# Kernel optimization log

Measured on AMD Instinct MI355X. Metric: run time of the kernel, lower is better.

Reference implementation:

```python
import jax, jax.numpy as jnp
import numpy as np

NMS_SIGMA = 2.0
MASK_THRESH = 0.5
N = 500
H = W = 256
NUM_CLS = 80


def setup_inputs() -> dict:
    key = jax.random.key(0)
    k1, k2, k3 = jax.random.split(key, 3)
    mask_preds = jax.random.uniform(k1, (N, H, W), dtype=jnp.float32)
    cate_scores = jax.random.uniform(k2, (N,), dtype=jnp.float32)
    cate_labels = jax.random.randint(k3, (N,), 0, NUM_CLS, dtype=jnp.int32)
    return {"mask_preds": mask_preds, "cate_scores": cate_scores, "cate_labels": cate_labels}


def reference(mask_preds, cate_scores, cate_labels):
    n = mask_preds.shape[0]
    # binarize masks (SOLOv2 inference: seg_masks = seg_preds > mask_thresh)
    seg_masks = (mask_preds > MASK_THRESH).astype(mask_preds.dtype)  # [N,H,W]
    sum_masks = seg_masks.sum(axis=(1, 2))                           # [N]
    # mask scoring: average soft score inside the binary mask
    seg_scores = (mask_preds * seg_masks).sum(axis=(1, 2)) / jnp.maximum(sum_masks, 1.0)
    scores = cate_scores * seg_scores                                # [N]
    # sort descending by score (matrix-NMS assumes sorted order)
    order = jnp.argsort(-scores)
    scores = scores[order]
    labels = cate_labels[order]
    flat = seg_masks[order].reshape(n, -1)                           # [N,HW]
    sums = sum_masks[order]
    # pairwise mask IoU, upper-triangular (j suppressed by i<j)
    inter = flat @ flat.T                                            # [N,N]
    union = sums[:, None] + sums[None, :] - inter
    iou = jnp.triu(inter / jnp.maximum(union, 1.0), k=1)
    label_match = jnp.triu((labels[:, None] == labels[None, :]).astype(iou.dtype), k=1)
    decay_iou = iou * label_match                                    # [N,N]
    # gaussian matrix-NMS decay
    compensate_iou = decay_iou.max(axis=0)                           # [N]
    decay_matrix = jnp.exp(-NMS_SIGMA * (decay_iou ** 2 - compensate_iou[:, None] ** 2))
    coeff = decay_matrix.min(axis=0)                                 # [N]
    updated_scores = scores * coeff
    return updated_scores
```

## Files before the change

kernel.cpp:

```cpp
#include <hip/hip_runtime.h>
#include <cstdint>

typedef unsigned long long u64;

#define THRESH 0.5f
#define SIGMA 2.0f

#define TPB 64
#define NSPLIT 8
#define CH 64
#define CST 66

__global__ __launch_bounds__(256) void k_pack_score(
    const float* __restrict__ preds, u64* __restrict__ packed,
    double* __restrict__ pssum, int* __restrict__ pcnt, int HW)
{
    const int b = blockIdx.x;
    const int i = b >> 2, sub = b & 3;
    const int seg = HW >> 2;
    const float* src = preds + (size_t)i * HW + (size_t)sub * seg;
    u64* dst = packed + (size_t)i * (HW >> 6) + (size_t)sub * (seg >> 6);
    const int tid = threadIdx.x;
    const int wave = tid >> 6, lane = tid & 63;
    double ssum = 0.0;
    int cnt = 0;
    const int iters = seg >> 10;
    for (int k = 0; k < iters; ++k) {
        const int p = (k << 10) + (wave << 8) + (lane << 2);
        const float4 v = *reinterpret_cast<const float4*>(src + p);
        const bool b0 = v.x > THRESH, b1 = v.y > THRESH, b2 = v.z > THRESH, b3 = v.w > THRESH;
        const u64 m0 = __ballot(b0);
        const u64 m1 = __ballot(b1);
        const u64 m2 = __ballot(b2);
        const u64 m3 = __ballot(b3);
        if (lane < 4) {
            const u64 m = (lane == 0) ? m0 : (lane == 1) ? m1 : (lane == 2) ? m2 : m3;
            dst[(k << 4) + (wave << 2) + lane] = m;
        }
        cnt += (int)b0 + (int)b1 + (int)b2 + (int)b3;
        ssum += (b0 ? (double)v.x : 0.0) + (b1 ? (double)v.y : 0.0)
              + (b2 ? (double)v.z : 0.0) + (b3 ? (double)v.w : 0.0);
    }
    for (int off = 32; off > 0; off >>= 1) {
        ssum += __shfl_down(ssum, off);
        cnt  += __shfl_down(cnt, off);
    }
    __shared__ double ls[4];
    __shared__ int lc[4];
    if (lane == 0) { ls[wave] = ssum; lc[wave] = cnt; }
    __syncthreads();
    if (tid == 0) {
        pssum[b] = ls[0] + ls[1] + ls[2] + ls[3];
        pcnt[b]  = lc[0] + lc[1] + lc[2] + lc[3];
    }
}

__global__ __launch_bounds__(512) void k_sort(
    const double* __restrict__ pssum, const int* __restrict__ pcnt,
    const float* __restrict__ cate, const int* __restrict__ labels,
    float* __restrict__ sScore, float* __restrict__ sSum,
    int* __restrict__ sLabel, int* __restrict__ order, int N)
{
    __shared__ float sc[512];
    const int i = threadIdx.x;
    float si = 0.f, su = 0.f;
    if (i < N) {
        const double S = pssum[4*i] + pssum[4*i+1] + pssum[4*i+2] + pssum[4*i+3];
        const int C = pcnt[4*i] + pcnt[4*i+1] + pcnt[4*i+2] + pcnt[4*i+3];
        si = cate[i] * (float)(S / (double)(C > 1 ? C : 1));
        su = (float)C;
        sc[i] = si;
    }
    __syncthreads();
    if (i < N) {
        int r = 0;
        for (int j = 0; j < N; ++j) {
            const float sj = sc[j];
            r += (sj > si) || (sj == si && j < i);
        }
        order[r] = i;
        sScore[r] = si;
        sSum[r] = su;
        sLabel[r] = labels[i];
    }
}

__global__ __launch_bounds__(256) void k_inter(
    const u64* __restrict__ packed, const int* __restrict__ order,
    unsigned* __restrict__ interBuf, int N, int WORDS, int NT)
{
    __shared__ u64 sm[2 * TPB][CST];
    int b = blockIdx.x;
    int ti = 0, rowlen = NT;
    while (b >= rowlen) { b -= rowlen; ++ti; --rowlen; }
    const int tj = ti + b;
    const int kwords = WORDS / NSPLIT;
    const int kbase = blockIdx.y * kwords;

    const int tid = threadIdx.x;
    const int a = tid >> 4, bb = tid & 15;

    unsigned acc[4][4] = {};
    for (int c = 0; c < kwords / CH; ++c) {
        const int base = kbase + c * CH;
        for (int idx = tid; idx < 2 * TPB * (CH / 2); idx += 256) {
            const int ml = idx >> 5;
            const int w = (idx & 31) << 1;
            const int g = (ml < TPB) ? (ti * TPB + ml) : (tj * TPB + (ml - TPB));
            u64 x0 = 0, x1 = 0;
            if (g < N) {
                const u64* p = packed + (size_t)order[g] * WORDS + base + w;
                x0 = p[0];
                x1 = p[1];
            }
            sm[ml][w] = x0;
            sm[ml][w + 1] = x1;
        }
        __syncthreads();
        #pragma unroll 2
        for (int w = 0; w < CH; w += 2) {
            u64 pi0[4], pi1[4], pj0[4], pj1[4];
            #pragma unroll
            for (int t = 0; t < 4; ++t) { pi0[t] = sm[4*a + t][w]; pi1[t] = sm[4*a + t][w + 1]; }
            #pragma unroll
            for (int s = 0; s < 4; ++s) { pj0[s] = sm[TPB + 4*bb + s][w]; pj1[s] = sm[TPB + 4*bb + s][w + 1]; }
            #pragma unroll
            for (int t = 0; t < 4; ++t)
                #pragma unroll
                for (int s = 0; s < 4; ++s)
                    acc[t][s] += (unsigned)__popcll(pi0[t] & pj0[s])
                               + (unsigned)__popcll(pi1[t] & pj1[s]);
        }
        __syncthreads();
    }
    #pragma unroll
    for (int t = 0; t < 4; ++t)
        #pragma unroll
        for (int s = 0; s < 4; ++s) {
            const int gi = ti * TPB + 4*a + t;
            const int gj = tj * TPB + 4*bb + s;
            if (gj < N && gi < gj) atomicAdd(&interBuf[(size_t)gi * N + gj], acc[t][s]);
        }
}

__global__ __launch_bounds__(256) void k_comp(
    const unsigned* __restrict__ interBuf, const float* __restrict__ sSum,
    const int* __restrict__ sLabel, float* __restrict__ comp, int N)
{
    const int c = blockIdx.x;
    const int tid = threadIdx.x;
    const float suc = sSum[c];
    const int lc_ = sLabel[c];
    float m = 0.0f;
    for (int k = tid; k < c; k += 256) {
        if (sLabel[k] == lc_) {
            const float inter = (float)interBuf[(size_t)k * N + c];
            const float un = sSum[k] + suc - inter;
            m = fmaxf(m, inter / fmaxf(un, 1.0f));
        }
    }
    for (int off = 32; off > 0; off >>= 1) m = fmaxf(m, __shfl_down(m, off));
    __shared__ float lm[4];
    const int wave = tid >> 6, lane = tid & 63;
    if (lane == 0) lm[wave] = m;
    __syncthreads();
    if (tid == 0) comp[c] = fmaxf(fmaxf(lm[0], lm[1]), fmaxf(lm[2], lm[3]));
}

__global__ __launch_bounds__(256) void k_final(
    const unsigned* __restrict__ interBuf, const float* __restrict__ comp,
    const float* __restrict__ sSum, const int* __restrict__ sLabel,
    const float* __restrict__ sScore, float* __restrict__ out, int N)
{
    const int j = blockIdx.x;
    const int tid = threadIdx.x;
    const float suj = sSum[j];
    const int lj = sLabel[j];
    float m = -3.0e38f;
    for (int i = tid; i < N; i += 256) {
        const float ci = comp[i];
        float d = 0.0f;
        if (i < j && sLabel[i] == lj) {
            const float inter = (float)interBuf[(size_t)i * N + j];
            const float un = sSum[i] + suj - inter;
            d = inter / fmaxf(un, 1.0f);
        }
        m = fmaxf(m, d * d - ci * ci);
    }
    for (int off = 32; off > 0; off >>= 1) m = fmaxf(m, __shfl_down(m, off));
    __shared__ float lm[4];
    const int wave = tid >> 6, lane = tid & 63;
    if (lane == 0) lm[wave] = m;
    __syncthreads();
    if (tid == 0) {
        const float mm = fmaxf(fmaxf(lm[0], lm[1]), fmaxf(lm[2], lm[3]));
        out[j] = sScore[j] * expf(-SIGMA * mm);
    }
}

extern "C" void kernel_launch(void* const* d_in, const int* in_sizes, int n_in,
                              void* d_out, int out_size, void* d_ws, size_t ws_size,
                              hipStream_t stream)
{
    const float* preds  = (const float*)d_in[0];
    const float* cate   = (const float*)d_in[1];
    const int*   labels = (const int*)d_in[2];
    float* out = (float*)d_out;

    const int N = in_sizes[1];
    const int HW = in_sizes[0] / N;
    const int WORDS = HW >> 6;

    char* ws = (char*)d_ws;
    size_t off = 0;
    auto take = [&](size_t bytes) -> void* {
        void* p = ws + off;
        off = (off + bytes + 255) & ~(size_t)255;
        return p;
    };
    u64*      packed   = (u64*)     take((size_t)N * WORDS * sizeof(u64));
    double*   pssum    = (double*)  take((size_t)N * 4 * sizeof(double));
    int*      pcnt     = (int*)     take((size_t)N * 4 * sizeof(int));
    float*    sScore   = (float*)   take((size_t)N * sizeof(float));
    float*    sSum     = (float*)   take((size_t)N * sizeof(float));
    int*      sLabel   = (int*)     take((size_t)N * sizeof(int));
    int*      order    = (int*)     take((size_t)N * sizeof(int));
    float*    comp     = (float*)   take((size_t)N * sizeof(float));
    unsigned* interBuf = (unsigned*)take((size_t)N * N * sizeof(unsigned));
    (void)ws_size; (void)n_in; (void)out_size;

    hipMemsetAsync(interBuf, 0, (size_t)N * N * sizeof(unsigned), stream);

    k_pack_score<<<N * 4, 256, 0, stream>>>(preds, packed, pssum, pcnt, HW);

    k_sort<<<1, 512, 0, stream>>>(pssum, pcnt, cate, labels,
                                  sScore, sSum, sLabel, order, N);

    const int NT = (N + TPB - 1) / TPB;
    dim3 grid(NT * (NT + 1) / 2, NSPLIT);
    k_inter<<<grid, 256, 0, stream>>>(packed, order, interBuf, N, WORDS, NT);

    k_comp<<<N, 256, 0, stream>>>(interBuf, sSum, sLabel, comp, N);

    k_final<<<N, 256, 0, stream>>>(interBuf, comp, sSum, sLabel, sScore, out, N);
}
```

Baseline: 278.2 us.

## Drop sort kernel, compute rank implicitly, write split-K partials instead of atomics

The separate sort kernel is removed. Score and mask-sum computation is folded into a one-block-per-mask pack kernel, and each mask's rank is computed inside the final kernel by counting higher-scoring masks, so the output is scattered by rank. The intersection kernel now works on unsorted masks. It loads its whole K slice into shared memory at once, with 16 splits, using vectorized 128-bit LDS reads and a strided column mapping. It writes per-split partials instead of using atomics, which removes the memset. The comp and final kernels fold 16 partials per pair, which adds memory traffic for the partial buffer.

```diff
diff --git a/kernel.cpp b/kernel.cpp
--- a/kernel.cpp
+++ b/kernel.cpp
@@ -5,28 +5,29 @@
 
 #define THRESH 0.5f
 #define SIGMA 2.0f
-
 #define TPB 64
-#define NSPLIT 8
-#define CH 64
+#define NSPLIT 16
 #define CST 66
 
-__global__ __launch_bounds__(256) void k_pack_score(
-    const float* __restrict__ preds, u64* __restrict__ packed,
-    double* __restrict__ pssum, int* __restrict__ pcnt, int HW)
-{
-    const int b = blockIdx.x;
-    const int i = b >> 2, sub = b & 3;
-    const int seg = HW >> 2;
-    const float* src = preds + (size_t)i * HW + (size_t)sub * seg;
-    u64* dst = packed + (size_t)i * (HW >> 6) + (size_t)sub * (seg >> 6);
+__device__ __forceinline__ bool better(float sa, int a, float sb, int b) {
+    return (sa > sb) || (sa == sb && a < b);
+}
+
+__global__ __launch_bounds__(512) void k_pack(
+    const float* __restrict__ preds, const float* __restrict__ cate,
+    u64* __restrict__ packed, float* __restrict__ score, float* __restrict__ sum,
+    int HW)
+{
+    const int i = blockIdx.x;
+    const float* src = preds + (size_t)i * HW;
+    u64* dst = packed + (size_t)i * (HW >> 6);
     const int tid = threadIdx.x;
     const int wave = tid >> 6, lane = tid & 63;
     double ssum = 0.0;
     int cnt = 0;
-    const int iters = seg >> 10;
+    const int iters = HW >> 11;
     for (int k = 0; k < iters; ++k) {
-        const int p = (k << 10) + (wave << 8) + (lane << 2);
+        const int p = (k << 11) + (wave << 8) + (lane << 2);
         const float4 v = *reinterpret_cast<const float4*>(src + p);
         const bool b0 = v.x > THRESH, b1 = v.y > THRESH, b2 = v.z > THRESH, b3 = v.w > THRESH;
         const u64 m0 = __ballot(b0);
@@ -35,7 +36,7 @@
         const u64 m3 = __ballot(b3);
         if (lane < 4) {
             const u64 m = (lane == 0) ? m0 : (lane == 1) ? m1 : (lane == 2) ? m2 : m3;
-            dst[(k << 4) + (wave << 2) + lane] = m;
+            dst[(k << 5) + (wave << 2) + lane] = m;
         }
         cnt += (int)b0 + (int)b1 + (int)b2 + (int)b3;
         ssum += (b0 ? (double)v.x : 0.0) + (b1 ? (double)v.y : 0.0)
@@ -45,51 +46,24 @@
         ssum += __shfl_down(ssum, off);
         cnt  += __shfl_down(cnt, off);
     }
-    __shared__ double ls[4];
-    __shared__ int lc[4];
+    __shared__ double ls[8];
+    __shared__ int lc[8];
     if (lane == 0) { ls[wave] = ssum; lc[wave] = cnt; }
     __syncthreads();
     if (tid == 0) {
-        pssum[b] = ls[0] + ls[1] + ls[2] + ls[3];
-        pcnt[b]  = lc[0] + lc[1] + lc[2] + lc[3];
-    }
-}
-
-__global__ __launch_bounds__(512) void k_sort(
-    const double* __restrict__ pssum, const int* __restrict__ pcnt,
-    const float* __restrict__ cate, const int* __restrict__ labels,
-    float* __restrict__ sScore, float* __restrict__ sSum,
-    int* __restrict__ sLabel, int* __restrict__ order, int N)
-{
-    __shared__ float sc[512];
-    const int i = threadIdx.x;
-    float si = 0.f, su = 0.f;
-    if (i < N) {
-        const double S = pssum[4*i] + pssum[4*i+1] + pssum[4*i+2] + pssum[4*i+3];
-        const int C = pcnt[4*i] + pcnt[4*i+1] + pcnt[4*i+2] + pcnt[4*i+3];
-        si = cate[i] * (float)(S / (double)(C > 1 ? C : 1));
-        su = (float)C;
-        sc[i] = si;
-    }
-    __syncthreads();
-    if (i < N) {
-        int r = 0;
-        for (int j = 0; j < N; ++j) {
-            const float sj = sc[j];
-            r += (sj > si) || (sj == si && j < i);
-        }
-        order[r] = i;
-        sScore[r] = si;
-        sSum[r] = su;
-        sLabel[r] = labels[i];
+        double S = 0.0; int C = 0;
+        #pragma unroll
+        for (int w = 0; w < 8; ++w) { S += ls[w]; C += lc[w]; }
+        score[i] = cate[i] * (float)(S / (double)(C > 1 ? C : 1));
+        sum[i] = (float)C;
     }
 }
 
 __global__ __launch_bounds__(256) void k_inter(
-    const u64* __restrict__ packed, const int* __restrict__ order,
-    unsigned* __restrict__ interBuf, int N, int WORDS, int NT)
-{
-    __shared__ u64 sm[2 * TPB][CST];
+    const u64* __restrict__ packed, unsigned* __restrict__ part,
+    int N, int WORDS, int NT)
+{
+    __shared__ __align__(16) u64 sm[2 * TPB][CST];
     int b = blockIdx.x;
     int ti = 0, rowlen = NT;
     while (b >= rowlen) { b -= rowlen; ++ti; --rowlen; }
@@ -100,101 +74,130 @@
     const int tid = threadIdx.x;
     const int a = tid >> 4, bb = tid & 15;
 
+    const int half = kwords >> 1;
+    for (int idx = tid; idx < 2 * TPB * half; idx += 256) {
+        const int ml = idx / half;
+        const int w = (idx - ml * half) << 1;
+        const int g = (ml < TPB) ? (ti * TPB + ml) : (tj * TPB + (ml - TPB));
+        u64 x0 = 0, x1 = 0;
+        if (g < N) {
+            const u64* p = packed + (size_t)g * WORDS + kbase + w;
+            x0 = p[0];
+            x1 = p[1];
+        }
+        sm[ml][w] = x0;
+        sm[ml][w + 1] = x1;
+    }
+    __syncthreads();
+
     unsigned acc[4][4] = {};
-    for (int c = 0; c < kwords / CH; ++c) {
-        const int base = kbase + c * CH;
-        for (int idx = tid; idx < 2 * TPB * (CH / 2); idx += 256) {
-            const int ml = idx >> 5;
-            const int w = (idx & 31) << 1;
-            const int g = (ml < TPB) ? (ti * TPB + ml) : (tj * TPB + (ml - TPB));
-            u64 x0 = 0, x1 = 0;
-            if (g < N) {
-                const u64* p = packed + (size_t)order[g] * WORDS + base + w;
-                x0 = p[0];
-                x1 = p[1];
-            }
-            sm[ml][w] = x0;
-            sm[ml][w + 1] = x1;
-        }
-        __syncthreads();
-        #pragma unroll 2
-        for (int w = 0; w < CH; w += 2) {
-            u64 pi0[4], pi1[4], pj0[4], pj1[4];
+    #pragma unroll 4
+    for (int w = 0; w < kwords; w += 2) {
+        u64 pi0[4], pi1[4], pj0[4], pj1[4];
+        #pragma unroll
+        for (int t = 0; t < 4; ++t) {
+            const ulonglong2 q = *reinterpret_cast<const ulonglong2*>(&sm[4 * a + t][w]);
+            pi0[t] = q.x; pi1[t] = q.y;
+        }
+        #pragma unroll
+        for (int s = 0; s < 4; ++s) {
+            const ulonglong2 q = *reinterpret_cast<const ulonglong2*>(&sm[TPB + bb + 16 * s][w]);
+            pj0[s] = q.x; pj1[s] = q.y;
+        }
+        #pragma unroll
+        for (int t = 0; t < 4; ++t)
             #pragma unroll
-            for (int t = 0; t < 4; ++t) { pi0[t] = sm[4*a + t][w]; pi1[t] = sm[4*a + t][w + 1]; }
-            #pragma unroll
-            for (int s = 0; s < 4; ++s) { pj0[s] = sm[TPB + 4*bb + s][w]; pj1[s] = sm[TPB + 4*bb + s][w + 1]; }
-            #pragma unroll
-            for (int t = 0; t < 4; ++t)
-                #pragma unroll
-                for (int s = 0; s < 4; ++s)
-                    acc[t][s] += (unsigned)__popcll(pi0[t] & pj0[s])
-                               + (unsigned)__popcll(pi1[t] & pj1[s]);
-        }
-        __syncthreads();
+            for (int s = 0; s < 4; ++s)
+                acc[t][s] += (unsigned)__popcll(pi0[t] & pj0[s])
+                           + (unsigned)__popcll(pi1[t] & pj1[s]);
     }
     #pragma unroll
     for (int t = 0; t < 4; ++t)
         #pragma unroll
         for (int s = 0; s < 4; ++s) {
-            const int gi = ti * TPB + 4*a + t;
-            const int gj = tj * TPB + 4*bb + s;
-            if (gj < N && gi < gj) atomicAdd(&interBuf[(size_t)gi * N + gj], acc[t][s]);
-        }
+            const int gi = ti * TPB + 4 * a + t;
+            const int gj = tj * TPB + bb + 16 * s;
+            if (gj < N && gi < gj)
+                part[((size_t)gi * N + gj) * NSPLIT + blockIdx.y] = acc[t][s];
+        }
+}
+
+__device__ __forceinline__ unsigned fold16(const unsigned* __restrict__ p) {
+    const uint4* q = reinterpret_cast<const uint4*>(p);
+    unsigned s = 0;
+    #pragma unroll
+    for (int k = 0; k < 4; ++k) {
+        const uint4 v = q[k];
+        s += v.x + v.y + v.z + v.w;
+    }
+    return s;
 }
 
 __global__ __launch_bounds__(256) void k_comp(
-    const unsigned* __restrict__ interBuf, const float* __restrict__ sSum,
-    const int* __restrict__ sLabel, float* __restrict__ comp, int N)
-{
-    const int c = blockIdx.x;
-    const int tid = threadIdx.x;
-    const float suc = sSum[c];
-    const int lc_ = sLabel[c];
+    const unsigned* __restrict__ part, const float* __restrict__ score,
+    const float* __restrict__ sum, const int* __restrict__ labels,
+    float* __restrict__ comp, int N)
+{
+    const int bI = blockIdx.x;
+    const float sb = score[bI], sub = sum[bI];
+    const int lb = labels[bI];
+    const int tid = threadIdx.x;
     float m = 0.0f;
-    for (int k = tid; k < c; k += 256) {
-        if (sLabel[k] == lc_) {
-            const float inter = (float)interBuf[(size_t)k * N + c];
-            const float un = sSum[k] + suc - inter;
-            m = fmaxf(m, inter / fmaxf(un, 1.0f));
-        }
+    for (int a = tid; a < N; a += 256) {
+        if (a == bI || labels[a] != lb) continue;
+        const float sa = score[a];
+        if (!better(sa, a, sb, bI)) continue;
+        const int lo = a < bI ? a : bI, hi = a < bI ? bI : a;
+        const float inter = (float)fold16(part + ((size_t)lo * N + hi) * NSPLIT);
+        const float un = sum[a] + sub - inter;
+        m = fmaxf(m, inter / fmaxf(un, 1.0f));
     }
     for (int off = 32; off > 0; off >>= 1) m = fmaxf(m, __shfl_down(m, off));
     __shared__ float lm[4];
     const int wave = tid >> 6, lane = tid & 63;
     if (lane == 0) lm[wave] = m;
     __syncthreads();
-    if (tid == 0) comp[c] = fmaxf(fmaxf(lm[0], lm[1]), fmaxf(lm[2], lm[3]));
+    if (tid == 0) comp[bI] = fmaxf(fmaxf(lm[0], lm[1]), fmaxf(lm[2], lm[3]));
 }
 
 __global__ __launch_bounds__(256) void k_final(
-    const unsigned* __restrict__ interBuf, const float* __restrict__ comp,
-    const float* __restrict__ sSum, const int* __restrict__ sLabel,
-    const float* __restrict__ sScore, float* __restrict__ out, int N)
-{
-    const int j = blockIdx.x;
-    const int tid = threadIdx.x;
-    const float suj = sSum[j];
-    const int lj = sLabel[j];
+    const unsigned* __restrict__ part, const float* __restrict__ score,
+    const float* __restrict__ sum, const int* __restrict__ labels,
+    const float* __restrict__ comp, float* __restrict__ out, int N)
+{
+    const int bI = blockIdx.x;
+    const float sb = score[bI], sub = sum[bI];
+    const int lb = labels[bI];
+    const int tid = threadIdx.x;
     float m = -3.0e38f;
-    for (int i = tid; i < N; i += 256) {
-        const float ci = comp[i];
+    int r = 0;
+    for (int a = tid; a < N; a += 256) {
+        const float sa = score[a];
+        const bool bet = (a != bI) && better(sa, a, sb, bI);
+        r += (int)bet;
         float d = 0.0f;
-        if (i < j && sLabel[i] == lj) {
-            const float inter = (float)interBuf[(size_t)i * N + j];
-            const float un = sSum[i] + suj - inter;
+        if (bet && labels[a] == lb) {
+            const int lo = a < bI ? a : bI, hi = a < bI ? bI : a;
+            const float inter = (float)fold16(part + ((size_t)lo * N + hi) * NSPLIT);
+            const float un = sum[a] + sub - inter;
             d = inter / fmaxf(un, 1.0f);
         }
-        m = fmaxf(m, d * d - ci * ci);
-    }
-    for (int off = 32; off > 0; off >>= 1) m = fmaxf(m, __shfl_down(m, off));
+        const float ca = comp[a];
+        m = fmaxf(m, d * d - ca * ca);
+    }
+    for (int off = 32; off > 0; off >>= 1) {
+        m = fmaxf(m, __shfl_down(m, off));
+        r += __shfl_down(r, off);
+    }
     __shared__ float lm[4];
+    __shared__ int lr[4];
     const int wave = tid >> 6, lane = tid & 63;
-    if (lane == 0) lm[wave] = m;
+    if (lane == 0) { lm[wave] = m; lr[wave] = r; }
     __syncthreads();
     if (tid == 0) {
         const float mm = fmaxf(fmaxf(lm[0], lm[1]), fmaxf(lm[2], lm[3]));
-        out[j] = sScore[j] * expf(-SIGMA * mm);
+        const int rank = lr[0] + lr[1] + lr[2] + lr[3];
+        out[rank] = sb * expf(-SIGMA * mm);
     }
 }
 
@@ -218,29 +221,20 @@
         off = (off + bytes + 255) & ~(size_t)255;
         return p;
     };
-    u64*      packed   = (u64*)     take((size_t)N * WORDS * sizeof(u64));
-    double*   pssum    = (double*)  take((size_t)N * 4 * sizeof(double));
-    int*      pcnt     = (int*)     take((size_t)N * 4 * sizeof(int));
-    float*    sScore   = (float*)   take((size_t)N * sizeof(float));
-    float*    sSum     = (float*)   take((size_t)N * sizeof(float));
-    int*      sLabel   = (int*)     take((size_t)N * sizeof(int));
-    int*      order    = (int*)     take((size_t)N * sizeof(int));
-    float*    comp     = (float*)   take((size_t)N * sizeof(float));
-    unsigned* interBuf = (unsigned*)take((size_t)N * N * sizeof(unsigned));
+    u64*      packed = (u64*)     take((size_t)N * WORDS * sizeof(u64));
+    float*    score  = (float*)   take((size_t)N * sizeof(float));
+    float*    sum    = (float*)   take((size_t)N * sizeof(float));
+    float*    comp   = (float*)   take((size_t)N * sizeof(float));
+    unsigned* part   = (unsigned*)take((size_t)N * N * NSPLIT * sizeof(unsigned));
     (void)ws_size; (void)n_in; (void)out_size;
 
-    hipMemsetAsync(interBuf, 0, (size_t)N * N * sizeof(unsigned), stream);
-
-    k_pack_score<<<N * 4, 256, 0, stream>>>(preds, packed, pssum, pcnt, HW);
-
-    k_sort<<<1, 512, 0, stream>>>(pssum, pcnt, cate, labels,
-                                  sScore, sSum, sLabel, order, N);
+    k_pack<<<N, 512, 0, stream>>>(preds, cate, packed, score, sum, HW);
 
     const int NT = (N + TPB - 1) / TPB;
     dim3 grid(NT * (NT + 1) / 2, NSPLIT);
-    k_inter<<<grid, 256, 0, stream>>>(packed, order, interBuf, N, WORDS, NT);
-
-    k_comp<<<N, 256, 0, stream>>>(interBuf, sSum, sLabel, comp, N);
-
-    k_final<<<N, 256, 0, stream>>>(interBuf, comp, sSum, sLabel, sScore, out, N);
-}
+    k_inter<<<grid, 256, 0, stream>>>(packed, part, N, WORDS, NT);
+
+    k_comp<<<N, 256, 0, stream>>>(part, score, sum, labels, comp, N);
+
+    k_final<<<N, 256, 0, stream>>>(part, score, sum, labels, comp, out, N);
+}
```

Result: faster. 245.5 us (-11.7%).
